# Optimization experiments

Hardware: AMD Instinct MI355X
Metric: run time of the kernel (lower is better)

Reference implementation:

```python
import jax, jax.numpy as jnp
import numpy as np

GRID = 14
N_HEADS = 12
TOP_K = 32


def _valid_indices(grid):
    """Replicates create_locality_mask: cls row/col always valid; patch pairs
    valid iff Chebyshev distance on the grid <= 2 (includes diagonal)."""
    n = grid * grid + 1
    mask = np.zeros((n, n), dtype=bool)
    mask[0, :] = True
    mask[:, 0] = True
    idx = np.arange(grid * grid)
    r, c = idx // grid, idx % grid
    cheb = np.maximum(np.abs(r[:, None] - r[None, :]), np.abs(c[:, None] - c[None, :]))
    mask[1:, 1:] = cheb <= 2
    i_idx, j_idx = np.nonzero(mask)
    return jnp.asarray(i_idx, dtype=jnp.int32), jnp.asarray(j_idx, dtype=jnp.int32)

I_IDX, J_IDX = _valid_indices(GRID)  # nv = 4489 valid (query, key) pairs


def setup_inputs() -> dict:
    key = jax.random.key(0)
    ks = jax.random.split(key, 6)
    B, L, D = 32, GRID * GRID + 1, 768
    s = 0.02
    return {
        "x": jax.random.normal(ks[0], (B, L, D), jnp.float32),
        "W_q": jax.random.normal(ks[1], (D, D), jnp.float32) * s,
        "b_q": jnp.zeros((D,), jnp.float32),
        "W_k": jax.random.normal(ks[2], (D, D), jnp.float32) * s,
        "b_k": jnp.zeros((D,), jnp.float32),
        "W_v": jax.random.normal(ks[3], (D, D), jnp.float32) * s,
        "b_v": jnp.zeros((D,), jnp.float32),
        "W_o": jax.random.normal(ks[4], (D, D), jnp.float32) * s,
        "b_o": jnp.zeros((D,), jnp.float32),
        "log_sigma": jnp.zeros((), jnp.float32),  # sigma = 1.0
    }


def reference(x, W_q, b_q, W_k, b_k, W_v, b_v, W_o, b_o, log_sigma):
    B, L, D = x.shape
    H, dk = N_HEADS, D // N_HEADS

    def proj(W, b):
        y = jnp.einsum('bld,de->ble', x, W) + b
        return y.reshape(B, L, H, dk).transpose(0, 2, 1, 3)  # [B,H,L,dk]

    Q, K, V = proj(W_q, b_q), proj(W_k, b_k), proj(W_v, b_v)

    sigma_sq = jnp.exp(2.0 * log_sigma)
    # gather valid (i,j) pairs; nv pairs from the locality mask
    q_valid = Q[:, :, I_IDX, :]                       # [B,H,nv,dk]
    k_valid = K[:, :, J_IDX, :]                       # [B,H,nv,dk]
    dist_sq = jnp.sum((q_valid - k_valid) ** 2, axis=-1)  # [B,H,nv]
    scores_valid = (-0.5 / sigma_sq) * dist_sq

    neg_inf = jnp.array(-jnp.inf, x.dtype)
    scores = jnp.full((B, H, L, L), neg_inf, dtype=x.dtype)
    scores = scores.at[:, :, I_IDX, J_IDX].set(scores_valid)

    k_top = min(TOP_K, L)
    _, top_idx = jax.lax.top_k(scores, k_top)          # [B,H,L,k]
    bb = jnp.arange(B)[:, None, None, None]
    hh = jnp.arange(H)[None, :, None, None]
    nn = jnp.arange(L)[None, None, :, None]
    topk_mask = jnp.zeros((B, H, L, L), bool).at[bb, hh, nn, top_idx].set(True)

    final_mask = jnp.isfinite(scores) & topk_mask
    scores = jnp.where(final_mask, scores, neg_inf)
    weights = jax.nn.softmax(scores, axis=-1)          # [B,H,L,L]
    attention_mask = (weights > 1e-6).astype(x.dtype)

    consensus = jnp.einsum('bhij,bhjd->bhid', weights, V)
    consensus = consensus.transpose(0, 2, 1, 3).reshape(B, L, D)
    out = jnp.einsum('bld,de->ble', consensus, W_o) + b_o
    return out, weights, attention_mask
```

## Files before the change

### kernel.cpp

```cpp
#include <hip/hip_runtime.h>
#include <hip/hip_bf16.h>
#include <math.h>

#define GRIDN 14
#define L 197
#define H 12
#define DK 64
#define D 768
#define B 32
#define BL (B*L)
#define TOPK 32
#define NBH (B*H)
#define NROW (NBH*L)
#define QKV_ELEMS ((size_t)NROW*DK)
#define KSTR 68
#define KROWS 127

typedef __attribute__((ext_vector_type(8))) short short8;
typedef __attribute__((ext_vector_type(4))) float floatx4;

__device__ __forceinline__ void load_lds16(void* lds, const void* g) {
    __builtin_amdgcn_global_load_lds(
        (const __attribute__((address_space(1))) unsigned int*)g,
        (__attribute__((address_space(3))) unsigned int*)lds, 16, 0, 0);
}

__global__ __launch_bounds__(256)
void prep(const float* __restrict__ x,
          const float* __restrict__ Wq, const float* __restrict__ Wk,
          const float* __restrict__ Wv, const float* __restrict__ Wo,
          __hip_bfloat16* __restrict__ xh, __hip_bfloat16* __restrict__ xl,
          __hip_bfloat16* __restrict__ WqTh, __hip_bfloat16* __restrict__ WqTl,
          __hip_bfloat16* __restrict__ WkTh, __hip_bfloat16* __restrict__ WkTl,
          __hip_bfloat16* __restrict__ WvT,  __hip_bfloat16* __restrict__ WoT)
{
    const int z = blockIdx.z;
    if (z == 4) {
        int lin = (blockIdx.y * 24 + blockIdx.x) * 256 + threadIdx.x;
        for (int i = lin; i < BL * D / 4; i += 24 * 24 * 256) {
            float4 v = ((const float4*)x)[i];
            union { __hip_bfloat16 b[4]; short4 s; } hh, ll;
            float f[4] = {v.x, v.y, v.z, v.w};
            #pragma unroll
            for (int j = 0; j < 4; ++j) {
                __hip_bfloat16 h = __float2bfloat16(f[j]);
                hh.b[j] = h;
                ll.b[j] = __float2bfloat16(f[j] - __bfloat162float(h));
            }
            ((short4*)xh)[i] = hh.s;
            ((short4*)xl)[i] = ll.s;
        }
        return;
    }
    __shared__ float tile[32][33];
    const float* src = (z == 0) ? Wq : (z == 1) ? Wk : (z == 2) ? Wv : Wo;
    __hip_bfloat16* dh = (z == 0) ? WqTh : (z == 1) ? WkTh : (z == 2) ? WvT : WoT;
    __hip_bfloat16* dl = (z == 0) ? WqTl : (z == 1) ? WkTl : nullptr;
    const int k0 = blockIdx.y * 32, n0 = blockIdx.x * 32;
    const int tx = threadIdx.x & 31, ty = threadIdx.x >> 5;

    for (int r = ty; r < 32; r += 8)
        tile[r][tx] = src[(size_t)(k0 + r) * D + n0 + tx];
    __syncthreads();
    for (int r = ty; r < 32; r += 8) {
        float v = tile[tx][r];
        __hip_bfloat16 h = __float2bfloat16(v);
        dh[(size_t)(n0 + r) * D + k0 + tx] = h;
        if (dl) dl[(size_t)(n0 + r) * D + k0 + tx] =
            __float2bfloat16(v - __bfloat162float(h));
    }
}

__global__ __launch_bounds__(256)
void gemm_qkv(const __hip_bfloat16* __restrict__ xh, const __hip_bfloat16* __restrict__ xl,
              const __hip_bfloat16* __restrict__ Wqh, const __hip_bfloat16* __restrict__ Wql,
              const __hip_bfloat16* __restrict__ Wkh, const __hip_bfloat16* __restrict__ Wkl,
              const __hip_bfloat16* __restrict__ Wvh,
              const float* __restrict__ bq, const float* __restrict__ bk,
              const float* __restrict__ bv,
              float* __restrict__ Qb, float* __restrict__ Kb, float* __restrict__ Vb)
{
    __shared__ __attribute__((aligned(16))) __hip_bfloat16 Ash[128 * 32];
    __shared__ __attribute__((aligned(16))) __hip_bfloat16 Bsh[128 * 32];
    __shared__ __attribute__((aligned(16))) __hip_bfloat16 Asl[128 * 32];
    __shared__ __attribute__((aligned(16))) __hip_bfloat16 Bsl[128 * 32];

    const int grp = blockIdx.y / 6, nt = blockIdx.y % 6;
    const __hip_bfloat16 *Bth, *Btl; const float* bias; float* C;
    if (grp == 0)      { Bth = Wqh; Btl = Wql; bias = bq; C = Qb; }
    else if (grp == 1) { Bth = Wkh; Btl = Wkl; bias = bk; C = Kb; }
    else               { Bth = Wvh; Btl = nullptr; bias = bv; C = Vb; }
    const bool split = (grp < 2);

    const int tid = threadIdx.x;
    const int wave = tid >> 6, lane = tid & 63;
    const int quad = lane >> 4, l16 = lane & 15;
    const int m0 = blockIdx.x * 128, n0 = nt * 128;
    const int wm = (wave & 1) * 64, wn = (wave >> 1) * 64;

    floatx4 acc[4][4] = {};

    int s_r[2], s_cs[2];
    #pragma unroll
    for (int u = 0; u < 2; ++u) {
        int idx = tid + u * 256;
        s_r[u] = idx >> 2; s_cs[u] = idx & 3;
    }

    for (int k0 = 0; k0 < D; k0 += 32) {
        #pragma unroll
        for (int u = 0; u < 2; ++u) {
            int r = s_r[u];
            int csrc = s_cs[u] ^ ((r >> 1) & 3);
            int gm = m0 + r; if (gm >= BL) gm = BL - 1;
            size_t aoff = (size_t)gm * D + k0 + csrc * 8;
            size_t boff = (size_t)(n0 + r) * D + k0 + csrc * 8;
            int lds_off = (wave * 64 + u * 256) * 16;
            load_lds16((char*)Ash + lds_off, xh + aoff);
            load_lds16((char*)Bsh + lds_off, Bth + boff);
            if (split) {
                load_lds16((char*)Asl + lds_off, xl + aoff);
                load_lds16((char*)Bsl + lds_off, Btl + boff);
            }
        }
        __syncthreads();

        short8 ah[4], bh[4];
        #pragma unroll
        for (int a = 0; a < 4; ++a) {
            int r = wm + a * 16 + l16;
            int slot = (r << 2) + (quad ^ ((r >> 1) & 3));
            ah[a] = *(const short8*)((const char*)Ash + (slot << 4));
        }
        #pragma unroll
        for (int b2 = 0; b2 < 4; ++b2) {
            int r = wn + b2 * 16 + l16;
            int slot = (r << 2) + (quad ^ ((r >> 1) & 3));
            bh[b2] = *(const short8*)((const char*)Bsh + (slot << 4));
        }
        if (split) {
            short8 al[4], bl[4];
            #pragma unroll
            for (int a = 0; a < 4; ++a) {
                int r = wm + a * 16 + l16;
                int slot = (r << 2) + (quad ^ ((r >> 1) & 3));
                al[a] = *(const short8*)((const char*)Asl + (slot << 4));
            }
            #pragma unroll
            for (int b2 = 0; b2 < 4; ++b2) {
                int r = wn + b2 * 16 + l16;
                int slot = (r << 2) + (quad ^ ((r >> 1) & 3));
                bl[b2] = *(const short8*)((const char*)Bsl + (slot << 4));
            }
            #pragma unroll
            for (int a = 0; a < 4; ++a)
                #pragma unroll
                for (int b2 = 0; b2 < 4; ++b2) {
                    acc[a][b2] = __builtin_amdgcn_mfma_f32_16x16x32_bf16(
                        al[a], bh[b2], acc[a][b2], 0, 0, 0);
                    acc[a][b2] = __builtin_amdgcn_mfma_f32_16x16x32_bf16(
                        ah[a], bl[b2], acc[a][b2], 0, 0, 0);
                }
        }
        #pragma unroll
        for (int a = 0; a < 4; ++a)
            #pragma unroll
            for (int b2 = 0; b2 < 4; ++b2)
                acc[a][b2] = __builtin_amdgcn_mfma_f32_16x16x32_bf16(
                    ah[a], bh[b2], acc[a][b2], 0, 0, 0);
        __syncthreads();
    }

    #pragma unroll
    for (int b2 = 0; b2 < 4; ++b2) {
        int n = n0 + wn + b2 * 16 + l16;
        float bvv = bias[n];
        int hh = n >> 6, dd = n & 63;
        #pragma unroll
        for (int a = 0; a < 4; ++a) {
            #pragma unroll
            for (int r = 0; r < 4; ++r) {
                int m = m0 + wm + a * 16 + quad * 4 + r;
                if (m < BL) {
                    int bb = m / L, ll = m % L;
                    C[((((size_t)bb * H + hh) * L + ll) << 6) + dd] =
                        acc[a][b2][r] + bvv;
                }
            }
        }
    }
}

__global__ __launch_bounds__(256)
void gemm_o(const __hip_bfloat16* __restrict__ A,
            const __hip_bfloat16* __restrict__ Bt,
            const float* __restrict__ bias, float* __restrict__ C)
{
    __shared__ __attribute__((aligned(16))) __hip_bfloat16 As[128 * 32];
    __shared__ __attribute__((aligned(16))) __hip_bfloat16 Bts[128 * 32];

    const int tid = threadIdx.x;
    const int wave = tid >> 6, lane = tid & 63;
    const int quad = lane >> 4, l16 = lane & 15;
    const int m0 = blockIdx.x * 128, n0 = blockIdx.y * 128;
    const int wm = (wave & 1) * 64, wn = (wave >> 1) * 64;

    floatx4 acc[4][4] = {};

    int s_r[2], s_cs[2];
    #pragma unroll
    for (int u = 0; u < 2; ++u) {
        int idx = tid + u * 256;
        s_r[u] = idx >> 2; s_cs[u] = idx & 3;
    }

    for (int k0 = 0; k0 < D; k0 += 32) {
        #pragma unroll
        for (int u = 0; u < 2; ++u) {
            int r = s_r[u];
            int csrc = s_cs[u] ^ ((r >> 1) & 3);
            int gm = m0 + r; if (gm >= BL) gm = BL - 1;
            int lds_off = (wave * 64 + u * 256) * 16;
            load_lds16((char*)As + lds_off, A + (size_t)gm * D + k0 + csrc * 8);
            load_lds16((char*)Bts + lds_off, Bt + (size_t)(n0 + r) * D + k0 + csrc * 8);
        }
        __syncthreads();

        short8 af[4], bf[4];
        #pragma unroll
        for (int a = 0; a < 4; ++a) {
            int r = wm + a * 16 + l16;
            int slot = (r << 2) + (quad ^ ((r >> 1) & 3));
            af[a] = *(const short8*)((const char*)As + (slot << 4));
        }
        #pragma unroll
        for (int b2 = 0; b2 < 4; ++b2) {
            int r = wn + b2 * 16 + l16;
            int slot = (r << 2) + (quad ^ ((r >> 1) & 3));
            bf[b2] = *(const short8*)((const char*)Bts + (slot << 4));
        }
        #pragma unroll
        for (int a = 0; a < 4; ++a)
            #pragma unroll
            for (int b2 = 0; b2 < 4; ++b2)
                acc[a][b2] = __builtin_amdgcn_mfma_f32_16x16x32_bf16(
                    af[a], bf[b2], acc[a][b2], 0, 0, 0);
        __syncthreads();
    }

    #pragma unroll
    for (int b2 = 0; b2 < 4; ++b2) {
        int n = n0 + wn + b2 * 16 + l16;
        float bvv = bias[n];
        #pragma unroll
        for (int a = 0; a < 4; ++a) {
            #pragma unroll
            for (int r = 0; r < 4; ++r) {
                int m = m0 + wm + a * 16 + quad * 4 + r;
                if (m < BL) C[(size_t)m * D + n] = acc[a][b2][r] + bvv;
            }
        }
    }
}

__global__ __launch_bounds__(512)
void attn_patch(const float* __restrict__ Q, const float* __restrict__ Kg,
                const float* __restrict__ Vg, const float* __restrict__ logsig,
                float* __restrict__ wout, float* __restrict__ mout,
                __hip_bfloat16* __restrict__ cons)
{
    __shared__ __attribute__((aligned(16))) float KV[KROWS * KSTR];
    __shared__ float qbuf[8][64];
    __shared__ float wjW[99][32];
    __shared__ unsigned char wjJ[99][32];
    __shared__ unsigned int winA[L];
    __shared__ unsigned char joff[76];

    const int bh = blockIdx.x;
    const int yb = blockIdx.y;
    const int b = bh / H, h = bh % H;
    const int tid = threadIdx.x, wave = tid >> 6, lane = tid & 63;
    const int half = lane & 1;
    const float* Kp = Kg + (size_t)bh * L * DK;
    const float* Vp = Vg + (size_t)bh * L * DK;

    if (yb == 2) {
        float* clsbuf = KV;
        float* w0 = KV + 200;
        unsigned char* j0 = (unsigned char*)(KV + 232);
        if (tid < 64) qbuf[0][tid] = Q[(size_t)bh * L * DK + tid];
        __syncthreads();
        const float coefc = -0.5f * expf(-2.0f * logsig[0]);

        {
            int t = wave * 25 + (lane >> 1);
            bool valid = (lane >> 1) < 25 && t < L;
            float s = 0.f;
            if (valid) {
                const float4* kp = (const float4*)&Kp[(size_t)t * DK + (half << 5)];
                const float4* qp = (const float4*)&qbuf[0][half << 5];
                #pragma unroll
                for (int d4 = 0; d4 < 8; ++d4) {
                    float4 qv = qp[d4], kv = kp[d4];
                    float dx = qv.x - kv.x, dy = qv.y - kv.y;
                    float dz = qv.z - kv.z, dw = qv.w - kv.w;
                    s += dx * dx + dy * dy + dz * dz + dw * dw;
                }
            }
            s += __shfl_xor(s, 1);
            if (valid && !half) clsbuf[t] = coefc * s;
        }
        __syncthreads();

        if (wave == 0) {
            const size_t wb = (size_t)(bh * L) * L;
            float orig[4], cur[4]; int selb = 0;
            #pragma unroll
            for (int k = 0; k < 4; ++k) {
                int t = lane + (k << 6);
                float v = (t < L) ? clsbuf[t] : -INFINITY;
                orig[k] = v; cur[k] = v;
            }
            float gmax = -INFINITY;
            for (int it = 0; it < TOPK; ++it) {
                float bv = cur[0]; int bt = lane;
                #pragma unroll
                for (int k = 1; k < 4; ++k)
                    if (cur[k] > bv) { bv = cur[k]; bt = lane + (k << 6); }
                #pragma unroll
                for (int off = 32; off; off >>= 1) {
                    float ov = __shfl_xor(bv, off);
                    int   ot = __shfl_xor(bt, off);
                    if (ov > bv || (ov == bv && ot < bt)) { bv = ov; bt = ot; }
                }
                if (it == 0) gmax = bv;
                if ((bt & 63) == lane) { cur[bt >> 6] = -INFINITY; selb |= 1 << (bt >> 6); }
            }
            float zl = 0.f; float wk[4];
            #pragma unroll
            for (int k = 0; k < 4; ++k) {
                wk[k] = ((selb >> k) & 1) ? expf(orig[k] - gmax) : 0.f;
                zl += wk[k];
            }
            #pragma unroll
            for (int off = 32; off; off >>= 1) zl += __shfl_xor(zl, off);

            #pragma unroll
            for (int k = 0; k < 4; ++k) {
                int p = lane + (k << 6);
                if (p < L) {
                    float wv = wk[k] / zl;
                    wout[wb + p] = wv;
                    mout[wb + p] = (wv > 1e-6f) ? 1.f : 0.f;
                }
            }
            int slot = 0;
            #pragma unroll
            for (int k = 0; k < 4; ++k) {
                bool sel = (selb >> k) & 1;
                unsigned long long mk = __ballot(sel);
                if (sel) {
                    int tt = slot + (int)__popcll(mk & ((1ull << lane) - 1ull));
                    w0[tt] = wk[k] / zl;
                    j0[tt] = (unsigned char)(lane + (k << 6));
                }
                slot += (int)__popcll(mk);
            }
            float acc = 0.f;
            #pragma unroll
            for (int t2 = 0; t2 < 32; ++t2)
                acc += w0[t2] * Vp[(size_t)j0[t2] * DK + lane];
            cons[((size_t)b * L) * D + h * 64 + lane] = __float2bfloat16(acc);
        }
        return;
    }

    const int base_i = yb * 99;
    const int joffs = yb ? 70 : 0;

    if (tid >= 1 && tid < L) {
        int r = (tid - 1) / GRIDN, c = (tid - 1) % GRIDN;
        int r0 = r - 2 < 0 ? 0 : r - 2, r1 = r + 2 > 13 ? 13 : r + 2;
        int c0 = c - 2 < 0 ? 0 : c - 2, c1 = c + 2 > 13 ? 13 : c + 2;
        int Wd = c1 - c0 + 1, Hh = r1 - r0 + 1;
        winA[tid] = (unsigned)r0 | ((unsigned)c0 << 8) |
                    ((unsigned)Wd << 16) | ((unsigned)Hh << 24);
    }
    if (tid < 75) {
        int w = tid / 25 + 3, tm = tid % 25;
        joff[tid] = (unsigned char)((tm / w) * GRIDN + tm % w);
    }

    int pr4[4], pc4[4];
    #pragma unroll
    for (int k = 0; k < 4; ++k) {
        int p = lane + (k << 6);
        if (p >= 1 && p < L) { pr4[k] = (p - 1) / GRIDN; pc4[k] = (p - 1) % GRIDN; }
        else                 { pr4[k] = 255; pc4[k] = 255; }
    }

    for (int idx = tid; idx < KROWS * 16; idx += 512) {
        int r = idx >> 4, c4 = idx & 15;
        int g = r ? r + joffs : 0;
        *(float4*)&KV[r * KSTR + c4 * 4] = *(const float4*)&Kp[g * 64 + c4 * 4];
    }
    __syncthreads();

    const float coef = -0.5f * expf(-2.0f * logsig[0]);
    const int starts0[9] = {1, 14, 27, 39, 51, 63, 75, 87, 99};
    const int starts1[9] = {99, 112, 124, 136, 148, 161, 173, 185, 197};
    const int i_begin = yb ? starts1[wave] : starts0[wave];
    const int i_end   = yb ? starts1[wave + 1] : starts0[wave + 1];

    float qreg = (i_begin < i_end)
               ? Q[((size_t)bh * L + i_begin) * 64 + lane] : 0.f;

    for (int i = i_begin; i < i_end; ++i) {
        const int rowid = bh * L + i;
        const size_t wb = (size_t)rowid * L;
        const int local = i - base_i;

        qbuf[wave][lane] = qreg;
        if (i + 1 < i_end)
            qreg = Q[((size_t)rowid + 1) * 64 + lane];

        const unsigned wa = winA[i];
        const int r0 = wa & 255, c0 = (wa >> 8) & 255;
        const int Wd2 = (wa >> 16) & 255, Hh = wa >> 24;
        const int n = Hh * Wd2 + 1;
        const int jbase = 1 + r0 * GRIDN + c0;

        int t = lane >> 1;
        bool valid = t < n;
        float s = 0.f; int j = 0;
        if (valid) {
            if (t > 0) j = jbase + joff[(Wd2 - 3) * 25 + (t - 1)];
            int js = j ? j - joffs : 0;
            const float4* kp = (const float4*)&KV[js * KSTR + (half << 5)];
            const float4* qp = (const float4*)&qbuf[wave][half << 5];
            #pragma unroll
            for (int d4 = 0; d4 < 8; ++d4) {
                float4 qv = qp[d4], kv = kp[d4];
                float dx = qv.x - kv.x, dy = qv.y - kv.y;
                float dz = qv.z - kv.z, dw = qv.w - kv.w;
                s += dx * dx + dy * dy + dz * dz + dw * dw;
            }
            j = js;
        }
        s += __shfl_xor(s, 1);
        float sc = valid ? coef * s : -INFINITY;

        float mx = sc;
        #pragma unroll
        for (int off = 32; off; off >>= 1) mx = fmaxf(mx, __shfl_xor(mx, off));
        float e = valid ? expf(sc - mx) : 0.f;
        float es = half ? 0.f : e;
        #pragma unroll
        for (int off = 32; off; off >>= 1) es += __shfl_xor(es, off);
        float wv = e / es;

        if (!half) {
            float wcv = valid ? wv : 0.f;
            wjW[local][t] = wcv;
            wjJ[local][t] = (unsigned char)(valid ? j : 0);
        }
        #pragma unroll
        for (int k = 0; k < 4; ++k) {
            int p = lane + (k << 6);
            if (p < L) {
                float wd = 0.f;
                if (p == 0) wd = wjW[local][0];
                else {
                    unsigned du = (unsigned)(pr4[k] - r0);
                    unsigned dv = (unsigned)(pc4[k] - c0);
                    if (du < (unsigned)Hh && dv < (unsigned)Wd2)
                        wd = wjW[local][1 + du * Wd2 + dv];
                }
                wout[wb + p] = wd;
                mout[wb + p] = (wd > 1e-6f) ? 1.f : 0.f;
            }
        }
    }
    __syncthreads();

    for (int idx = tid; idx < KROWS * 16; idx += 512) {
        int r = idx >> 4, c4 = idx & 15;
        int g = r ? r + joffs : 0;
        *(float4*)&KV[r * KSTR + c4 * 4] = *(const float4*)&Vp[g * 64 + c4 * 4];
    }
    __syncthreads();

    const int c_begin = yb ? starts1[wave] : starts0[wave];
    const int c_end   = yb ? starts1[wave + 1] : starts0[wave + 1];

    for (int i = c_begin; i < c_end; ++i) {
        const int local = i - base_i;
        float acc = 0.f;
        #pragma unroll
        for (int t = 0; t < 32; ++t) {
            float w = wjW[local][t];
            int j = wjJ[local][t];
            acc += w * KV[j * KSTR + lane];
        }
        cons[((size_t)b * L + i) * D + h * 64 + lane] = __float2bfloat16(acc);
    }
}

extern "C" void kernel_launch(void* const* d_in, const int* in_sizes, int n_in,
                              void* d_out, int out_size, void* d_ws, size_t ws_size,
                              hipStream_t stream)
{
    const float* x   = (const float*)d_in[0];
    const float* Wq  = (const float*)d_in[1];
    const float* bq  = (const float*)d_in[2];
    const float* Wk  = (const float*)d_in[3];
    const float* bk  = (const float*)d_in[4];
    const float* Wv  = (const float*)d_in[5];
    const float* bv  = (const float*)d_in[6];
    const float* Wo  = (const float*)d_in[7];
    const float* bo  = (const float*)d_in[8];
    const float* lsg = (const float*)d_in[9];

    float* out  = (float*)d_out;
    float* wout = out + QKV_ELEMS;
    float* mout = wout + (size_t)B * H * L * L;

    float* Qb  = (float*)d_ws;
    float* Kb  = Qb + QKV_ELEMS;
    float* Vb  = Kb + QKV_ELEMS;
    __hip_bfloat16* xh = (__hip_bfloat16*)(Vb + QKV_ELEMS);
    __hip_bfloat16* xl = xh + (size_t)BL * D;
    __hip_bfloat16* WqTh = xl + (size_t)BL * D;
    __hip_bfloat16* WqTl = WqTh + (size_t)D * D;
    __hip_bfloat16* WkTh = WqTl + (size_t)D * D;
    __hip_bfloat16* WkTl = WkTh + (size_t)D * D;
    __hip_bfloat16* WvT  = WkTl + (size_t)D * D;
    __hip_bfloat16* WoT  = WvT  + (size_t)D * D;
    __hip_bfloat16* consb = xh;

    prep<<<dim3(24, 24, 5), 256, 0, stream>>>(
        x, Wq, Wk, Wv, Wo, xh, xl, WqTh, WqTl, WkTh, WkTl, WvT, WoT);

    gemm_qkv<<<dim3(50, 18), 256, 0, stream>>>(
        xh, xl, WqTh, WqTl, WkTh, WkTl, WvT, bq, bk, bv, Qb, Kb, Vb);

    attn_patch<<<dim3(NBH, 3), 512, 0, stream>>>(
        Qb, Kb, Vb, lsg, wout, mout, consb);

    gemm_o<<<dim3(50, 6), 256, 0, stream>>>(consb, WoT, bo, out);
}
```

Baseline: 329.1 us.

## Double-buffer LDS in projection GEMMs and split QKV into QK and V kernels

Adds two-stage LDS double buffering to the QKV and output GEMMs, so global-to-LDS loads for the next K tile are issued before computing on the current one, hiding load latency. The combined QKV kernel, which branched between the split-precision Q/K path and the plain V path, is split into a gemm_qk kernel (always split-precision) and a separate gemm_v kernel. This removes divergent per-block work imbalance, at the cost of an extra launch and doubled LDS use, which may lower occupancy. There is also a possible race: the single sync per iteration does not wait for the async LDS loads into the next buffer to complete.

```diff
diff --git a/kernel.cpp b/kernel.cpp
--- a/kernel.cpp
+++ b/kernel.cpp
@@ -72,25 +72,22 @@
 }
 
 __global__ __launch_bounds__(256)
-void gemm_qkv(const __hip_bfloat16* __restrict__ xh, const __hip_bfloat16* __restrict__ xl,
-              const __hip_bfloat16* __restrict__ Wqh, const __hip_bfloat16* __restrict__ Wql,
-              const __hip_bfloat16* __restrict__ Wkh, const __hip_bfloat16* __restrict__ Wkl,
-              const __hip_bfloat16* __restrict__ Wvh,
-              const float* __restrict__ bq, const float* __restrict__ bk,
-              const float* __restrict__ bv,
-              float* __restrict__ Qb, float* __restrict__ Kb, float* __restrict__ Vb)
+void gemm_qk(const __hip_bfloat16* __restrict__ xh, const __hip_bfloat16* __restrict__ xl,
+             const __hip_bfloat16* __restrict__ Wqh, const __hip_bfloat16* __restrict__ Wql,
+             const __hip_bfloat16* __restrict__ Wkh, const __hip_bfloat16* __restrict__ Wkl,
+             const float* __restrict__ bq, const float* __restrict__ bk,
+             float* __restrict__ Qb, float* __restrict__ Kb)
 {
-    __shared__ __attribute__((aligned(16))) __hip_bfloat16 Ash[128 * 32];
-    __shared__ __attribute__((aligned(16))) __hip_bfloat16 Bsh[128 * 32];
-    __shared__ __attribute__((aligned(16))) __hip_bfloat16 Asl[128 * 32];
-    __shared__ __attribute__((aligned(16))) __hip_bfloat16 Bsl[128 * 32];
+    __shared__ __attribute__((aligned(16))) __hip_bfloat16 Ash[2][128 * 32];
+    __shared__ __attribute__((aligned(16))) __hip_bfloat16 Bsh[2][128 * 32];
+    __shared__ __attribute__((aligned(16))) __hip_bfloat16 Asl[2][128 * 32];
+    __shared__ __attribute__((aligned(16))) __hip_bfloat16 Bsl[2][128 * 32];
 
     const int grp = blockIdx.y / 6, nt = blockIdx.y % 6;
-    const __hip_bfloat16 *Bth, *Btl; const float* bias; float* C;
-    if (grp == 0)      { Bth = Wqh; Btl = Wql; bias = bq; C = Qb; }
-    else if (grp == 1) { Bth = Wkh; Btl = Wkl; bias = bk; C = Kb; }
-    else               { Bth = Wvh; Btl = nullptr; bias = bv; C = Vb; }
-    const bool split = (grp < 2);
+    const __hip_bfloat16* Bth = grp ? Wkh : Wqh;
+    const __hip_bfloat16* Btl = grp ? Wkl : Wql;
+    const float* bias = grp ? bk : bq;
+    float* C = grp ? Kb : Qb;
 
     const int tid = threadIdx.x;
     const int wave = tid >> 6, lane = tid & 63;
@@ -107,68 +104,57 @@
         s_r[u] = idx >> 2; s_cs[u] = idx & 3;
     }
 
-    for (int k0 = 0; k0 < D; k0 += 32) {
+    auto STAGE = [&](int buf, int kk) {
         #pragma unroll
         for (int u = 0; u < 2; ++u) {
             int r = s_r[u];
             int csrc = s_cs[u] ^ ((r >> 1) & 3);
             int gm = m0 + r; if (gm >= BL) gm = BL - 1;
-            size_t aoff = (size_t)gm * D + k0 + csrc * 8;
-            size_t boff = (size_t)(n0 + r) * D + k0 + csrc * 8;
+            size_t aoff = (size_t)gm * D + kk + csrc * 8;
+            size_t boff = (size_t)(n0 + r) * D + kk + csrc * 8;
             int lds_off = (wave * 64 + u * 256) * 16;
-            load_lds16((char*)Ash + lds_off, xh + aoff);
-            load_lds16((char*)Bsh + lds_off, Bth + boff);
-            if (split) {
-                load_lds16((char*)Asl + lds_off, xl + aoff);
-                load_lds16((char*)Bsl + lds_off, Btl + boff);
-            }
-        }
-        __syncthreads();
-
-        short8 ah[4], bh[4];
+            load_lds16((char*)Ash[buf] + lds_off, xh + aoff);
+            load_lds16((char*)Bsh[buf] + lds_off, Bth + boff);
+            load_lds16((char*)Asl[buf] + lds_off, xl + aoff);
+            load_lds16((char*)Bsl[buf] + lds_off, Btl + boff);
+        }
+    };
+
+    STAGE(0, 0);
+    __syncthreads();
+    int cur = 0;
+
+    for (int k0 = 0; k0 < D; k0 += 32) {
+        if (k0 + 32 < D) STAGE(cur ^ 1, k0 + 32);
+
+        short8 ah[4], bh[4], al[4], bl[4];
         #pragma unroll
         for (int a = 0; a < 4; ++a) {
             int r = wm + a * 16 + l16;
             int slot = (r << 2) + (quad ^ ((r >> 1) & 3));
-            ah[a] = *(const short8*)((const char*)Ash + (slot << 4));
+            ah[a] = *(const short8*)((const char*)Ash[cur] + (slot << 4));
+            al[a] = *(const short8*)((const char*)Asl[cur] + (slot << 4));
         }
         #pragma unroll
         for (int b2 = 0; b2 < 4; ++b2) {
             int r = wn + b2 * 16 + l16;
             int slot = (r << 2) + (quad ^ ((r >> 1) & 3));
-            bh[b2] = *(const short8*)((const char*)Bsh + (slot << 4));
-        }
-        if (split) {
-            short8 al[4], bl[4];
-            #pragma unroll
-            for (int a = 0; a < 4; ++a) {
-                int r = wm + a * 16 + l16;
-                int slot = (r << 2) + (quad ^ ((r >> 1) & 3));
-                al[a] = *(const short8*)((const char*)Asl + (slot << 4));
-            }
+            bh[b2] = *(const short8*)((const char*)Bsh[cur] + (slot << 4));
+            bl[b2] = *(const short8*)((const char*)Bsl[cur] + (slot << 4));
+        }
+        #pragma unroll
+        for (int a = 0; a < 4; ++a)
             #pragma unroll
             for (int b2 = 0; b2 < 4; ++b2) {
-                int r = wn + b2 * 16 + l16;
-                int slot = (r << 2) + (quad ^ ((r >> 1) & 3));
-                bl[b2] = *(const short8*)((const char*)Bsl + (slot << 4));
-            }
-            #pragma unroll
-            for (int a = 0; a < 4; ++a)
-                #pragma unroll
-                for (int b2 = 0; b2 < 4; ++b2) {
-                    acc[a][b2] = __builtin_amdgcn_mfma_f32_16x16x32_bf16(
-                        al[a], bh[b2], acc[a][b2], 0, 0, 0);
-                    acc[a][b2] = __builtin_amdgcn_mfma_f32_16x16x32_bf16(
-                        ah[a], bl[b2], acc[a][b2], 0, 0, 0);
-                }
-        }
-        #pragma unroll
-        for (int a = 0; a < 4; ++a)
-            #pragma unroll
-            for (int b2 = 0; b2 < 4; ++b2)
+                acc[a][b2] = __builtin_amdgcn_mfma_f32_16x16x32_bf16(
+                    al[a], bh[b2], acc[a][b2], 0, 0, 0);
+                acc[a][b2] = __builtin_amdgcn_mfma_f32_16x16x32_bf16(
+                    ah[a], bl[b2], acc[a][b2], 0, 0, 0);
                 acc[a][b2] = __builtin_amdgcn_mfma_f32_16x16x32_bf16(
                     ah[a], bh[b2], acc[a][b2], 0, 0, 0);
+            }
         __syncthreads();
+        cur ^= 1;
     }
 
     #pragma unroll
@@ -192,12 +178,12 @@
 }
 
 __global__ __launch_bounds__(256)
-void gemm_o(const __hip_bfloat16* __restrict__ A,
-            const __hip_bfloat16* __restrict__ Bt,
-            const float* __restrict__ bias, float* __restrict__ C)
+void gemm_v(const __hip_bfloat16* __restrict__ xh,
+            const __hip_bfloat16* __restrict__ Wvh,
+            const float* __restrict__ bv, float* __restrict__ Vb)
 {
-    __shared__ __attribute__((aligned(16))) __hip_bfloat16 As[128 * 32];
-    __shared__ __attribute__((aligned(16))) __hip_bfloat16 Bts[128 * 32];
+    __shared__ __attribute__((aligned(16))) __hip_bfloat16 As[2][128 * 32];
+    __shared__ __attribute__((aligned(16))) __hip_bfloat16 Bs[2][128 * 32];
 
     const int tid = threadIdx.x;
     const int wave = tid >> 6, lane = tid & 63;
@@ -214,30 +200,37 @@
         s_r[u] = idx >> 2; s_cs[u] = idx & 3;
     }
 
-    for (int k0 = 0; k0 < D; k0 += 32) {
+    auto STAGE = [&](int buf, int kk) {
         #pragma unroll
         for (int u = 0; u < 2; ++u) {
             int r = s_r[u];
             int csrc = s_cs[u] ^ ((r >> 1) & 3);
             int gm = m0 + r; if (gm >= BL) gm = BL - 1;
             int lds_off = (wave * 64 + u * 256) * 16;
-            load_lds16((char*)As + lds_off, A + (size_t)gm * D + k0 + csrc * 8);
-            load_lds16((char*)Bts + lds_off, Bt + (size_t)(n0 + r) * D + k0 + csrc * 8);
-        }
-        __syncthreads();
+            load_lds16((char*)As[buf] + lds_off, xh + (size_t)gm * D + kk + csrc * 8);
+            load_lds16((char*)Bs[buf] + lds_off, Wvh + (size_t)(n0 + r) * D + kk + csrc * 8);
+        }
+    };
+
+    STAGE(0, 0);
+    __syncthreads();
+    int cur = 0;
+
+    for (int k0 = 0; k0 < D; k0 += 32) {
+        if (k0 + 32 < D) STAGE(cur ^ 1, k0 + 32);
 
         short8 af[4], bf[4];
         #pragma unroll
         for (int a = 0; a < 4; ++a) {
             int r = wm + a * 16 + l16;
             int slot = (r << 2) + (quad ^ ((r >> 1) & 3));
-            af[a] = *(const short8*)((const char*)As + (slot << 4));
+            af[a] = *(const short8*)((const char*)As[cur] + (slot << 4));
         }
         #pragma unroll
         for (int b2 = 0; b2 < 4; ++b2) {
             int r = wn + b2 * 16 + l16;
             int slot = (r << 2) + (quad ^ ((r >> 1) & 3));
-            bf[b2] = *(const short8*)((const char*)Bts + (slot << 4));
+            bf[b2] = *(const short8*)((const char*)Bs[cur] + (slot << 4));
         }
         #pragma unroll
         for (int a = 0; a < 4; ++a)
@@ -246,6 +239,92 @@
                 acc[a][b2] = __builtin_amdgcn_mfma_f32_16x16x32_bf16(
                     af[a], bf[b2], acc[a][b2], 0, 0, 0);
         __syncthreads();
+        cur ^= 1;
+    }
+
+    #pragma unroll
+    for (int b2 = 0; b2 < 4; ++b2) {
+        int n = n0 + wn + b2 * 16 + l16;
+        float bvv = bv[n];
+        int hh = n >> 6, dd = n & 63;
+        #pragma unroll
+        for (int a = 0; a < 4; ++a) {
+            #pragma unroll
+            for (int r = 0; r < 4; ++r) {
+                int m = m0 + wm + a * 16 + quad * 4 + r;
+                if (m < BL) {
+                    int bb = m / L, ll = m % L;
+                    Vb[((((size_t)bb * H + hh) * L + ll) << 6) + dd] =
+                        acc[a][b2][r] + bvv;
+                }
+            }
+        }
+    }
+}
+
+__global__ __launch_bounds__(256)
+void gemm_o(const __hip_bfloat16* __restrict__ A,
+            const __hip_bfloat16* __restrict__ Bt,
+            const float* __restrict__ bias, float* __restrict__ C)
+{
+    __shared__ __attribute__((aligned(16))) __hip_bfloat16 As[2][128 * 32];
+    __shared__ __attribute__((aligned(16))) __hip_bfloat16 Bts[2][128 * 32];
+
+    const int tid = threadIdx.x;
+    const int wave = tid >> 6, lane = tid & 63;
+    const int quad = lane >> 4, l16 = lane & 15;
+    const int m0 = blockIdx.x * 128, n0 = blockIdx.y * 128;
+    const int wm = (wave & 1) * 64, wn = (wave >> 1) * 64;
+
+    floatx4 acc[4][4] = {};
+
+    int s_r[2], s_cs[2];
+    #pragma unroll
+    for (int u = 0; u < 2; ++u) {
+        int idx = tid + u * 256;
+        s_r[u] = idx >> 2; s_cs[u] = idx & 3;
+    }
+
+    auto STAGE = [&](int buf, int kk) {
+        #pragma unroll
+        for (int u = 0; u < 2; ++u) {
+            int r = s_r[u];
+            int csrc = s_cs[u] ^ ((r >> 1) & 3);
+            int gm = m0 + r; if (gm >= BL) gm = BL - 1;
+            int lds_off = (wave * 64 + u * 256) * 16;
+            load_lds16((char*)As[buf] + lds_off, A + (size_t)gm * D + kk + csrc * 8);
+            load_lds16((char*)Bts[buf] + lds_off, Bt + (size_t)(n0 + r) * D + kk + csrc * 8);
+        }
+    };
+
+    STAGE(0, 0);
+    __syncthreads();
+    int cur = 0;
+
+    for (int k0 = 0; k0 < D; k0 += 32) {
+        if (k0 + 32 < D) STAGE(cur ^ 1, k0 + 32);
+
+        short8 af[4], bf[4];
+        #pragma unroll
+        for (int a = 0; a < 4; ++a) {
+            int r = wm + a * 16 + l16;
+            int slot = (r << 2) + (quad ^ ((r >> 1) & 3));
+            af[a] = *(const short8*)((const char*)As[cur] + (slot << 4));
+        }
+        #pragma unroll
+        for (int b2 = 0; b2 < 4; ++b2) {
+            int r = wn + b2 * 16 + l16;
+            int slot = (r << 2) + (quad ^ ((r >> 1) & 3));
+            bf[b2] = *(const short8*)((const char*)Bts[cur] + (slot << 4));
+        }
+        #pragma unroll
+        for (int a = 0; a < 4; ++a)
+            #pragma unroll
+            for (int b2 = 0; b2 < 4; ++b2)
+                acc[a][b2] = __builtin_amdgcn_mfma_f32_16x16x32_bf16(
+                    af[a], bf[b2], acc[a][b2], 0, 0, 0);
+        __syncthreads();
+        cur ^= 1;
     }
 
     #pragma unroll
@@ -541,8 +620,11 @@
     prep<<<dim3(24, 24, 5), 256, 0, stream>>>(
         x, Wq, Wk, Wv, Wo, xh, xl, WqTh, WqTl, WkTh, WkTl, WvT, WoT);
 
-    gemm_qkv<<<dim3(50, 18), 256, 0, stream>>>(
-        xh, xl, WqTh, WqTl, WkTh, WkTl, WvT, bq, bk, bv, Qb, Kb, Vb);
+    gemm_qk<<<dim3(50, 12), 256, 0, stream>>>(
+        xh, xl, WqTh, WqTl, WkTh, WkTl, bq, bk, Qb, Kb);
+
+    gemm_v<<<dim3(50, 6), 256, 0, stream>>>(
+        xh, WvT, bv, Vb);
 
     attn_patch<<<dim3(NBH, 3), 512, 0, stream>>>(
         Qb, Kb, Vb, lsg, wout, mout, consb);
```

Result: slower. 357.6 us (+8.7%).
